# Kernel tuning notes

Hardware: AMD Instinct MI355X
Metric: run time of the kernel (lower is better)

## Reference

```python
import jax, jax.numpy as jnp
import numpy as np

# ---- static config (from init_kwargs) ----
CANVAS = (4, 32, 32)        # (C1, C2, C3) latent video canvas
TILE = (4, 8, 8)            # (T1, T2, T3) tile dims
KERNEL = (1, 3, 3)          # sliding kernel in tile units
ROPE_DIMS = (16, 56, 56)    # per-axis RoPE dims, sums to head_dim
THETA = 256.0
HEADS = 16
HEAD_DIM = 128
HIDDEN = HEADS * HEAD_DIM
B = 1
L = CANVAS[0] * CANVAS[1] * CANVAS[2]
EPS = 1e-6
SCALE = HEAD_DIM ** -0.5
D = tuple(CANVAS[i] // TILE[i] for i in range(3))   # tile grid (D1,D2,D3)
N_TILES = D[0] * D[1] * D[2]
T_TOK = TILE[0] * TILE[1] * TILE[2]


def _rope_tables():
    # 3D meshgrid positions, per-axis 1D rotary tables concatenated on feature dim
    grids = np.meshgrid(*[np.arange(c, dtype=np.float32) for c in CANVAS], indexing='ij')
    cos_l, sin_l = [], []
    for i in range(3):
        dim = ROPE_DIMS[i]
        freqs = 1.0 / (THETA ** (np.arange(0, dim, 2, dtype=np.float32) / dim))
        ang = grids[i].reshape(-1)[:, None] * freqs[None, :]          # [L, dim/2]
        cos_l.append(np.repeat(np.cos(ang), 2, axis=1))               # [L, dim]
        sin_l.append(np.repeat(np.sin(ang), 2, axis=1))
    return jnp.asarray(np.concatenate(cos_l, 1)), jnp.asarray(np.concatenate(sin_l, 1))


def _window_indices():
    # For each query tile (d1,d2,d3): attends to a clamped kernel window of kv tiles
    d1, d2, d3 = np.meshgrid(*[np.arange(d) for d in D], indexing='ij')
    idx = []
    for i, dg in enumerate((d1, d2, d3)):
        k = KERNEL[i]
        s = np.clip(dg - k // 2, 0, D[i] - k)                         # window start, [D1,D2,D3]
        shape = [1, 1, 1]
        shape[i] = k
        idx.append(s[..., None, None, None] + np.arange(k).reshape(shape))
    flat = (idx[0] * D[1] + idx[1]) * D[2] + idx[2]                   # [D1,D2,D3,k1,k2,k3]
    kt = KERNEL[0] * KERNEL[1] * KERNEL[2]
    return jnp.asarray(flat.reshape(N_TILES, kt))


def _tile(x):
    # [B,H,L,E] -> [B,H,N_tiles,T_tok,E] with (D1,T1,D2,T2,D3,T3) -> (D1,D2,D3,T1,T2,T3)
    b, h, _, e = x.shape
    x = x.reshape(b, h, D[0], TILE[0], D[1], TILE[1], D[2], TILE[2], e)
    x = x.transpose(0, 1, 2, 4, 6, 3, 5, 7, 8)
    return x.reshape(b, h, N_TILES, T_TOK, e)


def _untile(x):
    # inverse of _tile: [B,H,N_tiles,T_tok,E] -> [B,H,L,E]
    b, h, _, _, e = x.shape
    x = x.reshape(b, h, D[0], D[1], D[2], TILE[0], TILE[1], TILE[2], e)
    x = x.transpose(0, 1, 2, 5, 3, 6, 4, 7, 8)
    return x.reshape(b, h, L, e)


def _rms(x, g):
    return x * jax.lax.rsqrt(jnp.mean(x * x, axis=-1, keepdims=True) + EPS) * g


def _rope(x, cos, sin):
    # x: [B,L,H,E], cos/sin: [L,E]; rotate-half in interleaved pairs
    xr = x.reshape(*x.shape[:-1], HEAD_DIM // 2, 2)
    rot = jnp.stack([-xr[..., 1], xr[..., 0]], axis=-1).reshape(x.shape)
    return x * cos[None, :, None, :] + rot * sin[None, :, None, :]


def _forward(hidden_states, Wq, bq, Wk, bk, Wv, bv, Wo, bo, gq, gk):
    cos, sin = _rope_tables()
    q = hidden_states @ Wq + bq
    k = hidden_states @ Wk + bk
    v = hidden_states @ Wv + bv
    q = q.reshape(B, L, HEADS, HEAD_DIM)
    k = k.reshape(B, L, HEADS, HEAD_DIM)
    v = v.reshape(B, L, HEADS, HEAD_DIM)
    q = _rope(_rms(q, gq), cos, sin)
    k = _rope(_rms(k, gk), cos, sin)
    q = q.transpose(0, 2, 1, 3)  # [B,H,L,E]
    k = k.transpose(0, 2, 1, 3)
    v = v.transpose(0, 2, 1, 3)
    qt = _tile(q)                # [B,H,N,T,E]
    kt = _tile(k)
    vt = _tile(v)
    win = _window_indices()      # [N, Kt]
    kt_w = kt[:, :, win].reshape(B, HEADS, N_TILES, -1, HEAD_DIM)  # [B,H,N,Kt*T,E]
    vt_w = vt[:, :, win].reshape(B, HEADS, N_TILES, -1, HEAD_DIM)
    s = jnp.einsum('bhnqe,bhnke->bhnqk', qt, kt_w) * SCALE
    p = jax.nn.softmax(s, axis=-1)
    o = jnp.einsum('bhnqk,bhnke->bhnqe', p, vt_w)
    o = _untile(o).transpose(0, 2, 1, 3).reshape(B, L, HIDDEN)
    return o @ Wo + bo


def setup_inputs() -> dict:
    key = jax.random.key(0)
    ks = jax.random.split(key, 6)
    w = 0.02
    return {
        'hidden_states': jax.random.normal(ks[0], (B, L, HIDDEN), jnp.float32),
        'Wq': jax.random.normal(ks[1], (HIDDEN, HIDDEN), jnp.float32) * w,
        'bq': jnp.zeros((HIDDEN,), jnp.float32),
        'Wk': jax.random.normal(ks[2], (HIDDEN, HIDDEN), jnp.float32) * w,
        'bk': jnp.zeros((HIDDEN,), jnp.float32),
        'Wv': jax.random.normal(ks[3], (HIDDEN, HIDDEN), jnp.float32) * w,
        'bv': jnp.zeros((HIDDEN,), jnp.float32),
        'Wo': jax.random.normal(ks[4], (HIDDEN, HIDDEN), jnp.float32) * w,
        'bo': jnp.zeros((HIDDEN,), jnp.float32),
        'gq': jnp.ones((HEAD_DIM,), jnp.float32),
        'gk': jnp.ones((HEAD_DIM,), jnp.float32),
    }


def reference(hidden_states, Wq, bq, Wk, bk, Wv, bv, Wo, bo, gq, gk):
    return _forward(hidden_states, Wq, bq, Wk, bk, Wv, bv, Wo, bo, gq, gk)
```

## Files before the change

### kernel.cpp

```cpp
#include <hip/hip_runtime.h>
#include <math.h>

typedef __attribute__((ext_vector_type(8))) short bf16x8;
typedef __attribute__((ext_vector_type(4))) float f32x4;
typedef unsigned short u16;
typedef unsigned int u32;

#define N_TOK 4096
#define HID   2048
#define N_HEAD 16
#define HDIM  128
#define QK_SCALE 0.08838834764831845f
#define LOG2E_   1.4426950408889634f

__device__ __forceinline__ u16 f2bf(float x) {
  union { float f; u32 u; } v; v.f = x;
  u32 r = v.u + 0x7fffu + ((v.u >> 16) & 1u);
  return (u16)(r >> 16);
}

__device__ __forceinline__ void async16(const void* g, void* l) {
  __builtin_amdgcn_global_load_lds(
      (const __attribute__((address_space(1))) void*)g,
      (__attribute__((address_space(3))) void*)l, 16, 0, 0);
}

#define MFMA(a, b, c) __builtin_amdgcn_mfma_f32_16x16x32_bf16((a), (b), (c), 0, 0, 0)

__global__ void k_rope(float* __restrict__ cosT, float* __restrict__ sinT) {
  int l = blockIdx.x;
  int p = threadIdx.x;
  int c1 = l >> 10, c2 = (l >> 5) & 31, c3 = l & 31;
  int pos, j; float dim;
  if (p < 8)       { pos = c1; j = p;      dim = 16.f; }
  else if (p < 36) { pos = c2; j = p - 8;  dim = 56.f; }
  else             { pos = c3; j = p - 36; dim = 56.f; }
  float freq = exp2f(-8.0f * (2.0f * (float)j) / dim);
  float ang = (float)pos * freq;
  float s, c;
  sincosf(ang, &s, &c);
  cosT[l * 64 + p] = c;
  sinT[l * 64 + p] = s;
}

__global__ __launch_bounds__(256) void k_cvt_x(const float* __restrict__ X, u16* __restrict__ Xb) {
  int i = blockIdx.x * 256 + threadIdx.x;
  float4 v = ((const float4*)X)[i];
  ushort4 o;
  o.x = f2bf(v.x); o.y = f2bf(v.y); o.z = f2bf(v.z); o.w = f2bf(v.w);
  ((ushort4*)Xb)[i] = o;
}

__global__ __launch_bounds__(256) void k_tw(const float* __restrict__ Wq, const float* __restrict__ Wk,
                                            const float* __restrict__ Wv, const float* __restrict__ Wo,
                                            u16* __restrict__ WT) {
  int z = blockIdx.z;
  const float* W = (z == 0) ? Wq : (z == 1) ? Wk : (z == 2) ? Wv : Wo;
  u16* dst = WT + (size_t)z * 2048 * 2048;
  __shared__ __align__(16) float T[64][69];
  int n0 = blockIdx.x * 64, k0 = blockIdx.y * 64;
  int tid = threadIdx.x;
  int r = tid >> 4, c4 = tid & 15;
#pragma unroll
  for (int i = 0; i < 4; ++i) {
    int row = r + i * 16;
    float4 v = *(const float4*)(W + (size_t)(k0 + row) * 2048 + n0 + c4 * 4);
    T[row][c4 * 4 + 0] = v.x; T[row][c4 * 4 + 1] = v.y;
    T[row][c4 * 4 + 2] = v.z; T[row][c4 * 4 + 3] = v.w;
  }
  __syncthreads();
#pragma unroll
  for (int i = 0; i < 4; ++i) {
    int row = r + i * 16;
    ushort4 o;
    o.x = f2bf(T[c4 * 4 + 0][row]);
    o.y = f2bf(T[c4 * 4 + 1][row]);
    o.z = f2bf(T[c4 * 4 + 2][row]);
    o.w = f2bf(T[c4 * 4 + 3][row]);
    *(ushort4*)(dst + (size_t)(n0 + row) * 2048 + k0 + c4 * 4) = o;
  }
}

__global__ __launch_bounds__(256) void k_gemm(const u16* __restrict__ A, const u16* __restrict__ Bt,
                                              const float* __restrict__ bias, float* __restrict__ C,
                                              int M, int N, int K) {
  __shared__ __align__(16) char lds[2][2][16384];
  int nbn = N >> 7;
  int nwg = gridDim.x;
  int wg = (int)blockIdx.x;
  int cpx = nwg >> 3;
  wg = (wg & 7) * cpx + (wg >> 3);
  int bm = wg / nbn, bn = wg - bm * nbn;
  int tid = threadIdx.x;
  int lane = tid & 63, wid = tid >> 6;
  int g = lane >> 4, cl = lane & 15;
  int wm = (wid >> 1) * 64, wn = (wid & 1) * 64;
  const char* Ab0 = (const char*)A + (size_t)bm * 128 * (size_t)(K * 2);
  const char* Bb0 = (const char*)Bt + (size_t)bn * 128 * (size_t)(K * 2);
  int nk = K >> 6;

  f32x4 acc[4][4] = {};

  auto stage = [&](int buf, int kt) {
    const char* Ab = Ab0 + kt * 128;
    const char* Bb = Bb0 + kt * 128;
    char* La = &lds[buf][0][0];
    char* Lb = &lds[buf][1][0];
#pragma unroll
    for (int i = 0; i < 4; ++i) {
      int flat = tid + 256 * i;
      int row = flat >> 3, sb = flat & 7;
      async16(Ab + (size_t)row * (K * 2) + ((sb ^ (row & 7)) << 4), La + flat * 16);
    }
#pragma unroll
    for (int i = 0; i < 4; ++i) {
      int flat = tid + 256 * i;
      int row = flat >> 3, sb = flat & 7;
      async16(Bb + (size_t)row * (K * 2) + ((sb ^ (row & 7)) << 4), Lb + flat * 16);
    }
  };

  stage(0, 0);
  __syncthreads();
  for (int kt = 0; kt < nk; ++kt) {
    int cur = kt & 1;
    if (kt + 1 < nk) stage(cur ^ 1, kt + 1);
    const char* La = &lds[cur][0][0];
    const char* Lb = &lds[cur][1][0];
#pragma unroll
    for (int ks = 0; ks < 2; ++ks) {
      bf16x8 af[4], bfr[4];
#pragma unroll
      for (int mf = 0; mf < 4; ++mf) {
        int row = wm + mf * 16 + cl;
        af[mf] = *(const bf16x8*)(La + row * 128 + (((ks * 4 + g) ^ (row & 7)) << 4));
      }
#pragma unroll
      for (int nf = 0; nf < 4; ++nf) {
        int row = wn + nf * 16 + cl;
        bfr[nf] = *(const bf16x8*)(Lb + row * 128 + (((ks * 4 + g) ^ (row & 7)) << 4));
      }
#pragma unroll
      for (int mf = 0; mf < 4; ++mf)
#pragma unroll
        for (int nf = 0; nf < 4; ++nf)
          acc[mf][nf] = MFMA(af[mf], bfr[nf], acc[mf][nf]);
    }
    __syncthreads();
  }
#pragma unroll
  for (int mf = 0; mf < 4; ++mf)
#pragma unroll
    for (int nf = 0; nf < 4; ++nf) {
      int col = bn * 128 + wn + nf * 16 + cl;
      float b = bias[col];
#pragma unroll
      for (int r = 0; r < 4; ++r) {
        int row = bm * 128 + wm + mf * 16 + g * 4 + r;
        C[(size_t)row * N + col] = acc[mf][nf][r] + b;
      }
    }
}

__global__ __launch_bounds__(256) void k_prep_qk(const float* __restrict__ src, const float* __restrict__ gg,
                                                 const float* __restrict__ cosT, const float* __restrict__ sinT,
                                                 u16* __restrict__ dst, int isk) {
  int job = blockIdx.x * 4 + (threadIdx.x >> 6);
  int lane = threadIdx.x & 63;
  int tok = job & 4095, h = job >> 12;
  const float* row = src + (size_t)tok * 2048 + h * 128;
  float2 x = *(const float2*)(row + lane * 2);
  float ss = x.x * x.x + x.y * x.y;
#pragma unroll
  for (int m = 1; m < 64; m <<= 1) ss += __shfl_xor(ss, m, 64);
  float rms = rsqrtf(ss * (1.0f / 128.0f) + 1e-6f);
  float x0 = x.x * rms * gg[lane * 2];
  float x1 = x.y * rms * gg[lane * 2 + 1];
  float c = cosT[tok * 64 + lane], s = sinT[tok * 64 + lane];
  float y0 = x0 * c - x1 * s;
  float y1 = x1 * c + x0 * s;
  if (!isk) { y0 *= QK_SCALE * LOG2E_; y1 *= QK_SCALE * LOG2E_; }
  u32 pk = (u32)f2bf(y0) | ((u32)f2bf(y1) << 16);
  int c1 = tok >> 10, c2 = (tok >> 5) & 31, c3 = tok & 31;
  int n = (c2 >> 3) * 4 + (c3 >> 3);
  int t = c1 * 64 + (c2 & 7) * 8 + (c3 & 7);
  size_t rowidx = (size_t)(h * 16 + n) * 256 + t;
  if (!isk) {
    ((u32*)dst)[rowidx * 64 + lane] = pk;
  } else {
    char* base = (char*)dst + rowidx * 256;
    *(u32*)(base + ((((lane >> 2) ^ (t & 7)) << 4) + (lane & 3) * 4)) = pk;
  }
}

__global__ __launch_bounds__(256) void k_prep_v(const float* __restrict__ src, u16* __restrict__ Vt) {
  __shared__ __align__(16) u16 T[128][72];
  int tid = threadIdx.x;
  int h = blockIdx.x >> 6, n = (blockIdx.x >> 2) & 15, ch = blockIdx.x & 3;
  int d2 = n >> 2, d3 = n & 3;
  int tc = tid >> 2, cq = tid & 3;
  int tok = (ch * 32 + d2 * 8 + (tc >> 3)) * 32 + d3 * 8 + (tc & 7);
  const float* sp = src + (size_t)tok * 2048 + h * 128;
#pragma unroll
  for (int i = 0; i < 8; ++i) {
    int d0 = cq * 4 + i * 16;
    float4 v = *(const float4*)(sp + d0);
    T[d0 + 0][tc] = f2bf(v.x); T[d0 + 1][tc] = f2bf(v.y);
    T[d0 + 2][tc] = f2bf(v.z); T[d0 + 3][tc] = f2bf(v.w);
  }
  __syncthreads();
  int d = tid >> 1, half = tid & 1;
  char* dstb = (char*)Vt + ((size_t)((h * 16 + n) * 4 + ch) * 128 + d) * 128;
#pragma unroll
  for (int b = 0; b < 4; ++b) {
    int blk = half * 4 + b;
    uint4 val = *(const uint4*)&T[d][blk * 8];
    *(uint4*)(dstb + ((blk ^ (d & 7)) << 4)) = val;
  }
}

__global__ __launch_bounds__(512) void k_attn(const u16* __restrict__ Qt, const u16* __restrict__ Kt,
                                              const u16* __restrict__ Vt, u16* __restrict__ AO) {
  __shared__ __align__(16) char Kl[2][16384];
  __shared__ __align__(16) char Vl[2][16384];
  __shared__ __align__(16) char Pl[8][4096];
  int tid = threadIdx.x;
  int lane = tid & 63, wid = tid >> 6;
  int g = lane >> 4, cl = lane & 15;
  int h = blockIdx.x >> 4, n = blockIdx.x & 15;
  int d2 = n >> 2, d3 = n & 3;
  int s2 = d2 - 1; s2 = s2 < 0 ? 0 : (s2 > 1 ? 1 : s2);
  int s3 = d3 - 1; s3 = s3 < 0 ? 0 : (s3 > 1 ? 1 : s3);
  int q0 = wid * 32;

  bf16x8 qf[2][4];
  const char* Qb = (const char*)Qt + (size_t)(h * 16 + n) * 256 * 256;
#pragma unroll
  for (int nq = 0; nq < 2; ++nq)
#pragma unroll
    for (int kf = 0; kf < 4; ++kf)
      qf[nq][kf] = *(const bf16x8*)(Qb + (q0 + nq * 16 + cl) * 256 + kf * 64 + g * 16);

  f32x4 o[2][8] = {};
  float ms0 = -__builtin_inff(), ms1 = -__builtin_inff();
  float ls0 = 0.f, ls1 = 0.f;

  auto stage = [&](int buf, int c) {
    int kvi = c >> 2, cc = c & 3;
    int i2 = kvi / 3, i3 = kvi - i2 * 3;
    int kvt = (s2 + i2) * 4 + (s3 + i3);
    const char* Kb = (const char*)Kt + ((size_t)((h * 16 + kvt) * 256 + cc * 64)) * 256;
    const char* Vb = (const char*)Vt + ((size_t)((h * 16 + kvt) * 4 + cc)) * 16384;
#pragma unroll
    for (int i = 0; i < 2; ++i) {
      int flat = tid + 512 * i;
      async16(Kb + flat * 16, &Kl[buf][0] + flat * 16);
      async16(Vb + flat * 16, &Vl[buf][0] + flat * 16);
    }
  };

  stage(0, 0);
  __syncthreads();

  char* Pw = &Pl[wid][0];
  for (int c = 0; c < 36; ++c) {
    int cur = c & 1;
    if (c + 1 < 36) stage(cur ^ 1, c + 1);
    const char* Kc = &Kl[cur][0];
    f32x4 st[4][2] = {};
#pragma unroll
    for (int ks = 0; ks < 4; ++ks) {
      bf16x8 af[4];
#pragma unroll
      for (int mk = 0; mk < 4; ++mk) {
        int row = mk * 16 + cl;
        af[mk] = *(const bf16x8*)(Kc + row * 256 + (((ks * 4 + g) ^ (row & 7)) << 4));
      }
#pragma unroll
      for (int mk = 0; mk < 4; ++mk) {
        st[mk][0] = MFMA(af[mk], qf[0][ks], st[mk][0]);
        st[mk][1] = MFMA(af[mk], qf[1][ks], st[mk][1]);
      }
    }
    float al0, al1;
    {
      float cm = st[0][0][0];
#pragma unroll
      for (int mk = 0; mk < 4; ++mk)
#pragma unroll
        for (int r = 0; r < 4; ++r) cm = fmaxf(cm, st[mk][0][r]);
      cm = fmaxf(cm, __shfl_xor(cm, 16, 64));
      cm = fmaxf(cm, __shfl_xor(cm, 32, 64));
      float mn = fmaxf(ms0, cm);
      al0 = exp2f(ms0 - mn);
      float rs = 0.f;
#pragma unroll
      for (int mk = 0; mk < 4; ++mk)
#pragma unroll
        for (int r = 0; r < 4; ++r) {
          float p = exp2f(st[mk][0][r] - mn);
          st[mk][0][r] = p; rs += p;
        }
      rs += __shfl_xor(rs, 16, 64);
      rs += __shfl_xor(rs, 32, 64);
      ls0 = ls0 * al0 + rs; ms0 = mn;
    }
    {
      float cm = st[0][1][0];
#pragma unroll
      for (int mk = 0; mk < 4; ++mk)
#pragma unroll
        for (int r = 0; r < 4; ++r) cm = fmaxf(cm, st[mk][1][r]);
      cm = fmaxf(cm, __shfl_xor(cm, 16, 64));
      cm = fmaxf(cm, __shfl_xor(cm, 32, 64));
      float mn = fmaxf(ms1, cm);
      al1 = exp2f(ms1 - mn);
      float rs = 0.f;
#pragma unroll
      for (int mk = 0; mk < 4; ++mk)
#pragma unroll
        for (int r = 0; r < 4; ++r) {
          float p = exp2f(st[mk][1][r] - mn);
          st[mk][1][r] = p; rs += p;
        }
      rs += __shfl_xor(rs, 16, 64);
      rs += __shfl_xor(rs, 32, 64);
      ls1 = ls1 * al1 + rs; ms1 = mn;
    }
#pragma unroll
    for (int nq = 0; nq < 2; ++nq) {
      int q = nq * 16 + cl;
#pragma unroll
      for (int mk = 0; mk < 4; ++mk)
#pragma unroll
        for (int rp = 0; rp < 2; ++rp) {
          u32 pk = (u32)f2bf(st[mk][nq][rp * 2]) | ((u32)f2bf(st[mk][nq][rp * 2 + 1]) << 16);
          int kv = mk * 16 + g * 4 + rp * 2;
          *(u32*)(Pw + q * 128 + (((kv >> 3) ^ (q & 7)) << 4) + (kv & 7) * 2) = pk;
        }
    }
    float ar0[4], ar1[4];
#pragma unroll
    for (int r = 0; r < 4; ++r) {
      ar0[r] = __shfl(al0, g * 4 + r, 64);
      ar1[r] = __shfl(al1, g * 4 + r, 64);
    }
#pragma unroll
    for (int nd = 0; nd < 8; ++nd)
#pragma unroll
      for (int r = 0; r < 4; ++r) {
        o[0][nd][r] *= ar0[r];
        o[1][nd][r] *= ar1[r];
      }
    const char* Vc = &Vl[cur][0];
#pragma unroll
    for (int ks = 0; ks < 2; ++ks) {
      bf16x8 pf0, pf1, vf[8];
      {
        int q = cl;
        pf0 = *(const bf16x8*)(Pw + q * 128 + (((ks * 4 + g) ^ (q & 7)) << 4));
        q = 16 + cl;
        pf1 = *(const bf16x8*)(Pw + q * 128 + (((ks * 4 + g) ^ (q & 7)) << 4));
      }
#pragma unroll
      for (int nd = 0; nd < 8; ++nd) {
        int d = nd * 16 + cl;
        vf[nd] = *(const bf16x8*)(Vc + d * 128 + (((ks * 4 + g) ^ (d & 7)) << 4));
      }
#pragma unroll
      for (int nd = 0; nd < 8; ++nd) {
        o[0][nd] = MFMA(pf0, vf[nd], o[0][nd]);
        o[1][nd] = MFMA(pf1, vf[nd], o[1][nd]);
      }
    }
    __syncthreads();
  }
  float lr0[4], lr1[4];
#pragma unroll
  for (int r = 0; r < 4; ++r) {
    lr0[r] = 1.0f / __shfl(ls0, g * 4 + r, 64);
    lr1[r] = 1.0f / __shfl(ls1, g * 4 + r, 64);
  }
#pragma unroll
  for (int mo = 0; mo < 2; ++mo)
#pragma unroll
    for (int r = 0; r < 4; ++r) {
      int t = q0 + mo * 16 + g * 4 + r;
      int t1 = t >> 6, t2 = (t >> 3) & 7, t3 = t & 7;
      int tok = (t1 * 32 + d2 * 8 + t2) * 32 + d3 * 8 + t3;
      u16* orow = AO + (size_t)tok * HID + h * HDIM;
      float lr = (mo == 0) ? lr0[r] : lr1[r];
#pragma unroll
      for (int nd = 0; nd < 8; ++nd)
        orow[nd * 16 + cl] = f2bf(o[mo][nd][r] * lr);
    }
}

extern "C" void kernel_launch(void* const* d_in, const int* in_sizes, int n_in,
                              void* d_out, int out_size, void* d_ws, size_t ws_size,
                              hipStream_t stream) {
  const float* X  = (const float*)d_in[0];
  const float* Wq = (const float*)d_in[1];
  const float* bq = (const float*)d_in[2];
  const float* Wk = (const float*)d_in[3];
  const float* bk = (const float*)d_in[4];
  const float* Wv = (const float*)d_in[5];
  const float* bv = (const float*)d_in[6];
  const float* Wo = (const float*)d_in[7];
  const float* bo = (const float*)d_in[8];
  const float* gq = (const float*)d_in[9];
  const float* gk = (const float*)d_in[10];

  char* ws = (char*)d_ws;
  size_t off = 0;
  auto alloc = [&](size_t bytes) { void* p = ws + off; off = (off + bytes + 255) & ~(size_t)255; return p; };
  u16*   Xb   = (u16*)alloc((size_t)N_TOK * HID * 2);
  u16*   WT   = (u16*)alloc((size_t)4 * 2048 * 2048 * 2);
  float* PF   = (float*)alloc((size_t)N_TOK * HID * 4);
  float* COS  = (float*)alloc((size_t)N_TOK * 64 * 4);
  float* SIN  = (float*)alloc((size_t)N_TOK * 64 * 4);
  u16*   Qt   = (u16*)alloc((size_t)N_TOK * HID * 2);
  u16*   Kt   = (u16*)alloc((size_t)N_TOK * HID * 2);
  u16*   Vt   = (u16*)alloc((size_t)N_TOK * HID * 2);
  u16*   AO   = (u16*)alloc((size_t)N_TOK * HID * 2);
  float* OUT  = (float*)d_out;

  k_rope<<<N_TOK, 64, 0, stream>>>(COS, SIN);
  k_cvt_x<<<(N_TOK * HID / 4) / 256, 256, 0, stream>>>(X, Xb);
  k_tw<<<dim3(32, 32, 4), 256, 0, stream>>>(Wq, Wk, Wv, Wo, WT);

  k_gemm<<<512, 256, 0, stream>>>(Xb, WT + (size_t)0 * 2048 * 2048, bq, PF, 4096, 2048, 2048);
  k_prep_qk<<<16384, 256, 0, stream>>>(PF, gq, COS, SIN, Qt, 0);
  k_gemm<<<512, 256, 0, stream>>>(Xb, WT + (size_t)1 * 2048 * 2048, bk, PF, 4096, 2048, 2048);
  k_prep_qk<<<16384, 256, 0, stream>>>(PF, gk, COS, SIN, Kt, 1);
  k_gemm<<<512, 256, 0, stream>>>(Xb, WT + (size_t)2 * 2048 * 2048, bv, PF, 4096, 2048, 2048);
  k_prep_v<<<1024, 256, 0, stream>>>(PF, Vt);

  k_attn<<<256, 512, 0, stream>>>(Qt, Kt, Vt, AO);

  k_gemm<<<512, 256, 0, stream>>>(AO, WT + (size_t)3 * 2048 * 2048, bo, OUT, 4096, 2048, 2048);
}
```

Measured before the change: 450.5 us.

## Fuse QKV into pipelined 256x256 GEMM and simplify attention softmax

Measured after the change: 460.8 us. +2.3%, slower.

```diff
diff --git a/kernel.cpp b/kernel.cpp
--- a/kernel.cpp
+++ b/kernel.cpp
@@ -17,6 +17,12 @@
   union { float f; u32 u; } v; v.f = x;
   u32 r = v.u + 0x7fffu + ((v.u >> 16) & 1u);
   return (u16)(r >> 16);
+}
+
+__device__ __forceinline__ u32 cvtpk(float lo, float hi) {
+  u32 r;
+  asm("v_cvt_pk_bf16_f32 %0, %1, %2" : "=v"(r) : "v"(lo), "v"(hi));
+  return r;
 }
 
 __device__ __forceinline__ void async16(const void* g, void* l) {
@@ -81,94 +87,127 @@
   }
 }
 
-__global__ __launch_bounds__(256) void k_gemm(const u16* __restrict__ A, const u16* __restrict__ Bt,
-                                              const float* __restrict__ bias, float* __restrict__ C,
-                                              int M, int N, int K) {
-  __shared__ __align__(16) char lds[2][2][16384];
-  int nbn = N >> 7;
+
+#define VM8 asm volatile("s_waitcnt vmcnt(8)" ::: "memory");
+#define VM6 asm volatile("s_waitcnt vmcnt(6)" ::: "memory");
+#define VMNONE
+
+#define STAGEU(SB, SAB, SH, ST) do {                                            \
+    int st_ = (ST) < Tk ? (ST) : Tk - 1;                                        \
+    const char* src_ = ((SAB) ? Bp : Ap) + (size_t)((SH) * 128) * Kb + (size_t)st_ * 128; \
+    char* dstl_ = &Lds[SB][SAB][SH][0];                                         \
+    _Pragma("unroll")                                                           \
+    for (int i_ = 0; i_ < 2; ++i_) {                                            \
+      int flat_ = tid + 512 * i_;                                               \
+      int row_ = flat_ >> 3, sb_ = flat_ & 7;                                   \
+      async16(src_ + (size_t)row_ * Kb + ((sb_ ^ (row_ & 7)) << 4), dstl_ + flat_ * 16); \
+    }                                                                           \
+  } while (0)
+
+#define PHASE(BUF, MH, NH, READA, VMOP, SB, SAB, SH, ST) do {                   \
+    VMOP                                                                        \
+    __builtin_amdgcn_s_barrier();                                               \
+    asm volatile("" ::: "memory");                                              \
+    bf16x8 bb[2][2];                                                            \
+    const char* Lm = &Lds[BUF][0][MH][0];                                       \
+    const char* Ln = &Lds[BUF][1][NH][0];                                       \
+    if (READA) {                                                                \
+      _Pragma("unroll")                                                         \
+      for (int kk = 0; kk < 2; ++kk)                                            \
+        _Pragma("unroll")                                                       \
+        for (int mf = 0; mf < 4; ++mf) {                                        \
+          int row = wmIdx * 64 + mf * 16 + cl;                                  \
+          af[kk][mf] = *(const bf16x8*)(Lm + row * 128 + (((kk * 4 + g) ^ (row & 7)) << 4)); \
+        }                                                                       \
+    }                                                                           \
+    _Pragma("unroll")                                                           \
+    for (int kk = 0; kk < 2; ++kk)                                              \
+      _Pragma("unroll")                                                         \
+      for (int nf = 0; nf < 2; ++nf) {                                          \
+        int row = wnIdx * 32 + nf * 16 + cl;                                    \
+        bb[kk][nf] = *(const bf16x8*)(Ln + row * 128 + (((kk * 4 + g) ^ (row & 7)) << 4)); \
+      }                                                                         \
+    STAGEU(SB, SAB, SH, ST);                                                    \
+    __builtin_amdgcn_s_setprio(1);                                              \
+    _Pragma("unroll")                                                           \
+    for (int kk = 0; kk < 2; ++kk)                                              \
+      _Pragma("unroll")                                                         \
+      for (int mf = 0; mf < 4; ++mf)                                            \
+        _Pragma("unroll")                                                       \
+        for (int nf = 0; nf < 2; ++nf)                                          \
+          acc[(MH) * 4 + mf][(NH) * 2 + nf] =                                   \
+              MFMA(af[kk][mf], bb[kk][nf], acc[(MH) * 4 + mf][(NH) * 2 + nf]);  \
+    __builtin_amdgcn_s_setprio(0);                                              \
+  } while (0)
+
+__global__ __launch_bounds__(512, 2) void k_gemm8(const u16* __restrict__ A, const u16* __restrict__ Bt,
+                                                  const float* __restrict__ b0, const float* __restrict__ b1,
+                                                  const float* __restrict__ b2, float* __restrict__ C,
+                                                  int gn, int K, int ldc) {
+  __shared__ __align__(16) char Lds[2][2][2][16384];
+  int tid = threadIdx.x;
+  int lane = tid & 63, wid = tid >> 6;
+  int g = lane >> 4, cl = lane & 15;
+  int wmIdx = wid >> 2, wnIdx = wid & 3;
   int nwg = gridDim.x;
   int wg = (int)blockIdx.x;
   int cpx = nwg >> 3;
   wg = (wg & 7) * cpx + (wg >> 3);
-  int bm = wg / nbn, bn = wg - bm * nbn;
-  int tid = threadIdx.x;
-  int lane = tid & 63, wid = tid >> 6;
-  int g = lane >> 4, cl = lane & 15;
-  int wm = (wid >> 1) * 64, wn = (wid & 1) * 64;
-  const char* Ab0 = (const char*)A + (size_t)bm * 128 * (size_t)(K * 2);
-  const char* Bb0 = (const char*)Bt + (size_t)bn * 128 * (size_t)(K * 2);
-  int nk = K >> 6;
-
-  f32x4 acc[4][4] = {};
-
-  auto stage = [&](int buf, int kt) {
-    const char* Ab = Ab0 + kt * 128;
-    const char* Bb = Bb0 + kt * 128;
-    char* La = &lds[buf][0][0];
-    char* Lb = &lds[buf][1][0];
-#pragma unroll
-    for (int i = 0; i < 4; ++i) {
-      int flat = tid + 256 * i;
-      int row = flat >> 3, sb = flat & 7;
-      async16(Ab + (size_t)row * (K * 2) + ((sb ^ (row & 7)) << 4), La + flat * 16);
-    }
-#pragma unroll
-    for (int i = 0; i < 4; ++i) {
-      int flat = tid + 256 * i;
-      int row = flat >> 3, sb = flat & 7;
-      async16(Bb + (size_t)row * (K * 2) + ((sb ^ (row & 7)) << 4), Lb + flat * 16);
-    }
-  };
-
-  stage(0, 0);
-  __syncthreads();
-  for (int kt = 0; kt < nk; ++kt) {
-    int cur = kt & 1;
-    if (kt + 1 < nk) stage(cur ^ 1, kt + 1);
-    const char* La = &lds[cur][0][0];
-    const char* Lb = &lds[cur][1][0];
-#pragma unroll
-    for (int ks = 0; ks < 2; ++ks) {
-      bf16x8 af[4], bfr[4];
-#pragma unroll
-      for (int mf = 0; mf < 4; ++mf) {
-        int row = wm + mf * 16 + cl;
-        af[mf] = *(const bf16x8*)(La + row * 128 + (((ks * 4 + g) ^ (row & 7)) << 4));
-      }
-#pragma unroll
-      for (int nf = 0; nf < 4; ++nf) {
-        int row = wn + nf * 16 + cl;
-        bfr[nf] = *(const bf16x8*)(Lb + row * 128 + (((ks * 4 + g) ^ (row & 7)) << 4));
-      }
-#pragma unroll
-      for (int mf = 0; mf < 4; ++mf)
-#pragma unroll
-        for (int nf = 0; nf < 4; ++nf)
-          acc[mf][nf] = MFMA(af[mf], bfr[nf], acc[mf][nf]);
-    }
-    __syncthreads();
-  }
-#pragma unroll
-  for (int mf = 0; mf < 4; ++mf)
-#pragma unroll
-    for (int nf = 0; nf < 4; ++nf) {
-      int col = bn * 128 + wn + nf * 16 + cl;
-      float b = bias[col];
-#pragma unroll
-      for (int r = 0; r < 4; ++r) {
-        int row = bm * 128 + wm + mf * 16 + g * 4 + r;
-        C[(size_t)row * N + col] = acc[mf][nf][r] + b;
-      }
-    }
-}
-
-__global__ __launch_bounds__(256) void k_prep_qk(const float* __restrict__ src, const float* __restrict__ gg,
+  int bm = wg / gn, bn = wg % gn;
+  size_t Kb = (size_t)K * 2;
+  const char* Ap = (const char*)A + (size_t)bm * 256 * Kb;
+  const char* Bp = (const char*)Bt + (size_t)bn * 256 * Kb;
+  int Tk = K >> 6;
+
+  f32x4 acc[8][4] = {};
+  bf16x8 af[2][4];
+
+  STAGEU(0, 0, 0, 0);
+  STAGEU(0, 1, 0, 0);
+  STAGEU(0, 0, 1, 0);
+  STAGEU(0, 1, 1, 0);
+  STAGEU(1, 0, 0, 1);
+  STAGEU(1, 1, 0, 1);
+
+  int nIter = Tk >> 1;
+  for (int it = 0; it < nIter; ++it) {
+    int t = 2 * it;
+    PHASE(0, 0, 0, 1, VM8,    1, 0, 1, t + 1);
+    PHASE(0, 0, 1, 0, VM6,    1, 1, 1, t + 1);
+    PHASE(0, 1, 0, 1, VMNONE, 0, 0, 0, t + 2);
+    PHASE(0, 1, 1, 0, VMNONE, 0, 1, 0, t + 2);
+    PHASE(1, 0, 0, 1, VM8,    0, 0, 1, t + 2);
+    PHASE(1, 0, 1, 0, VM6,    0, 1, 1, t + 2);
+    PHASE(1, 1, 0, 1, VMNONE, 1, 0, 0, t + 3);
+    PHASE(1, 1, 1, 0, VMNONE, 1, 1, 0, t + 3);
+  }
+
+#pragma unroll
+  for (int mfp = 0; mfp < 8; ++mfp) {
+    int rowBase = (mfp < 4 ? wmIdx * 64 + mfp * 16 : 128 + wmIdx * 64 + (mfp - 4) * 16) + g * 4;
+    int rowG = bm * 256 + rowBase;
+#pragma unroll
+    for (int nfp = 0; nfp < 4; ++nfp) {
+      int colLoc = (nfp < 2 ? wnIdx * 32 + nfp * 16 : 128 + wnIdx * 32 + (nfp - 2) * 16) + cl;
+      int col = bn * 256 + colLoc;
+      int z = col >> 11;
+      const float* bp = (z == 0) ? b0 : (z == 1) ? b1 : b2;
+      float bv = bp[col & 2047];
+#pragma unroll
+      for (int rr = 0; rr < 4; ++rr)
+        C[(size_t)(rowG + rr) * ldc + col] = acc[mfp][nfp][rr] + bv;
+    }
+  }
+}
+
+__global__ __launch_bounds__(256) void k_prep_qk(const float* __restrict__ src, int stride,
+                                                 const float* __restrict__ gg,
                                                  const float* __restrict__ cosT, const float* __restrict__ sinT,
                                                  u16* __restrict__ dst, int isk) {
   int job = blockIdx.x * 4 + (threadIdx.x >> 6);
   int lane = threadIdx.x & 63;
   int tok = job & 4095, h = job >> 12;
-  const float* row = src + (size_t)tok * 2048 + h * 128;
+  const float* row = src + (size_t)tok * stride + h * 128;
   float2 x = *(const float2*)(row + lane * 2);
   float ss = x.x * x.x + x.y * x.y;
 #pragma unroll
@@ -180,7 +219,7 @@
   float y0 = x0 * c - x1 * s;
   float y1 = x1 * c + x0 * s;
   if (!isk) { y0 *= QK_SCALE * LOG2E_; y1 *= QK_SCALE * LOG2E_; }
-  u32 pk = (u32)f2bf(y0) | ((u32)f2bf(y1) << 16);
+  u32 pk = cvtpk(y0, y1);
   int c1 = tok >> 10, c2 = (tok >> 5) & 31, c3 = tok & 31;
   int n = (c2 >> 3) * 4 + (c3 >> 3);
   int t = c1 * 64 + (c2 & 7) * 8 + (c3 & 7);
@@ -193,14 +232,15 @@
   }
 }
 
-__global__ __launch_bounds__(256) void k_prep_v(const float* __restrict__ src, u16* __restrict__ Vt) {
+__global__ __launch_bounds__(256) void k_prep_v(const float* __restrict__ src, int stride,
+                                                u16* __restrict__ Vt) {
   __shared__ __align__(16) u16 T[128][72];
   int tid = threadIdx.x;
   int h = blockIdx.x >> 6, n = (blockIdx.x >> 2) & 15, ch = blockIdx.x & 3;
   int d2 = n >> 2, d3 = n & 3;
   int tc = tid >> 2, cq = tid & 3;
   int tok = (ch * 32 + d2 * 8 + (tc >> 3)) * 32 + d3 * 8 + (tc & 7);
-  const float* sp = src + (size_t)tok * 2048 + h * 128;
+  const float* sp = src + (size_t)tok * stride + h * 128;
 #pragma unroll
   for (int i = 0; i < 8; ++i) {
     int d0 = cq * 4 + i * 16;
@@ -227,7 +267,10 @@
   int tid = threadIdx.x;
   int lane = tid & 63, wid = tid >> 6;
   int g = lane >> 4, cl = lane & 15;
-  int h = blockIdx.x >> 4, n = blockIdx.x & 15;
+  int bid = (int)blockIdx.x;
+  int xcd = bid & 7, i = bid >> 3;
+  int h = xcd * 2 + (i >> 4);
+  int n = i & 15;
   int d2 = n >> 2, d3 = n & 3;
   int s2 = d2 - 1; s2 = s2 < 0 ? 0 : (s2 > 1 ? 1 : s2);
   int s3 = d3 - 1; s3 = s3 < 0 ? 0 : (s3 > 1 ? 1 : s3);
@@ -242,8 +285,7 @@
       qf[nq][kf] = *(const bf16x8*)(Qb + (q0 + nq * 16 + cl) * 256 + kf * 64 + g * 16);
 
   f32x4 o[2][8] = {};
-  float ms0 = -__builtin_inff(), ms1 = -__builtin_inff();
-  float ls0 = 0.f, ls1 = 0.f;
+  float L0 = 0.f, L1 = 0.f;
 
   auto stage = [&](int buf, int c) {
     int kvi = c >> 2, cc = c & 3;
@@ -252,8 +294,8 @@
     const char* Kb = (const char*)Kt + ((size_t)((h * 16 + kvt) * 256 + cc * 64)) * 256;
     const char* Vb = (const char*)Vt + ((size_t)((h * 16 + kvt) * 4 + cc)) * 16384;
 #pragma unroll
-    for (int i = 0; i < 2; ++i) {
-      int flat = tid + 512 * i;
+    for (int i_ = 0; i_ < 2; ++i_) {
+      int flat = tid + 512 * i_;
       async16(Kb + flat * 16, &Kl[buf][0] + flat * 16);
       async16(Vb + flat * 16, &Vl[buf][0] + flat * 16);
     }
@@ -268,6 +310,7 @@
     if (c + 1 < 36) stage(cur ^ 1, c + 1);
     const char* Kc = &Kl[cur][0];
     f32x4 st[4][2] = {};
+    __builtin_amdgcn_s_setprio(1);
 #pragma unroll
     for (int ks = 0; ks < 4; ++ks) {
       bf16x8 af[4];
@@ -282,51 +325,16 @@
         st[mk][1] = MFMA(af[mk], qf[1][ks], st[mk][1]);
       }
     }
-    float al0, al1;
-    {
-      float cm = st[0][0][0];
-#pragma unroll
-      for (int mk = 0; mk < 4; ++mk)
-#pragma unroll
-        for (int r = 0; r < 4; ++r) cm = fmaxf(cm, st[mk][0][r]);
-      cm = fmaxf(cm, __shfl_xor(cm, 16, 64));
-      cm = fmaxf(cm, __shfl_xor(cm, 32, 64));
-      float mn = fmaxf(ms0, cm);
-      al0 = exp2f(ms0 - mn);
-      float rs = 0.f;
-#pragma unroll
-      for (int mk = 0; mk < 4; ++mk)
-#pragma unroll
-        for (int r = 0; r < 4; ++r) {
-          float p = exp2f(st[mk][0][r] - mn);
-          st[mk][0][r] = p; rs += p;
-        }
-      rs += __shfl_xor(rs, 16, 64);
-      rs += __shfl_xor(rs, 32, 64);
-      ls0 = ls0 * al0 + rs; ms0 = mn;
-    }
-    {
-      float cm = st[0][1][0];
-#pragma unroll
-      for (int mk = 0; mk < 4; ++mk)
-#pragma unroll
-        for (int r = 0; r < 4; ++r) cm = fmaxf(cm, st[mk][1][r]);
-      cm = fmaxf(cm, __shfl_xor(cm, 16, 64));
-      cm = fmaxf(cm, __shfl_xor(cm, 32, 64));
-      float mn = fmaxf(ms1, cm);
-      al1 = exp2f(ms1 - mn);
-      float rs = 0.f;
-#pragma unroll
-      for (int mk = 0; mk < 4; ++mk)
-#pragma unroll
-        for (int r = 0; r < 4; ++r) {
-          float p = exp2f(st[mk][1][r] - mn);
-          st[mk][1][r] = p; rs += p;
-        }
-      rs += __shfl_xor(rs, 16, 64);
-      rs += __shfl_xor(rs, 32, 64);
-      ls1 = ls1 * al1 + rs; ms1 = mn;
-    }
+    __builtin_amdgcn_s_setprio(0);
+#pragma unroll
+    for (int mk = 0; mk < 4; ++mk)
+#pragma unroll
+      for (int r = 0; r < 4; ++r) {
+        float p0 = exp2f(st[mk][0][r]);
+        float p1 = exp2f(st[mk][1][r]);
+        st[mk][0][r] = p0; L0 += p0;
+        st[mk][1][r] = p1; L1 += p1;
+      }
 #pragma unroll
     for (int nq = 0; nq < 2; ++nq) {
       int q = nq * 16 + cl;
@@ -334,25 +342,13 @@
       for (int mk = 0; mk < 4; ++mk)
 #pragma unroll
         for (int rp = 0; rp < 2; ++rp) {
-          u32 pk = (u32)f2bf(st[mk][nq][rp * 2]) | ((u32)f2bf(st[mk][nq][rp * 2 + 1]) << 16);
+          u32 pk = cvtpk(st[mk][nq][rp * 2], st[mk][nq][rp * 2 + 1]);
           int kv = mk * 16 + g * 4 + rp * 2;
           *(u32*)(Pw + q * 128 + (((kv >> 3) ^ (q & 7)) << 4) + (kv & 7) * 2) = pk;
         }
     }
-    float ar0[4], ar1[4];
-#pragma unroll
-    for (int r = 0; r < 4; ++r) {
-      ar0[r] = __shfl(al0, g * 4 + r, 64);
-      ar1[r] = __shfl(al1, g * 4 + r, 64);
-    }
-#pragma unroll
-    for (int nd = 0; nd < 8; ++nd)
-#pragma unroll
-      for (int r = 0; r < 4; ++r) {
-        o[0][nd][r] *= ar0[r];
-        o[1][nd][r] *= ar1[r];
-      }
     const char* Vc = &Vl[cur][0];
+    __builtin_amdgcn_s_setprio(1);
 #pragma unroll
     for (int ks = 0; ks < 2; ++ks) {
       bf16x8 pf0, pf1, vf[8];
@@ -373,13 +369,16 @@
         o[1][nd] = MFMA(pf1, vf[nd], o[1][nd]);
       }
     }
+    __builtin_amdgcn_s_setprio(0);
     __syncthreads();
   }
+  L0 += __shfl_xor(L0, 16, 64); L0 += __shfl_xor(L0, 32, 64);
+  L1 += __shfl_xor(L1, 16, 64); L1 += __shfl_xor(L1, 32, 64);
   float lr0[4], lr1[4];
 #pragma unroll
   for (int r = 0; r < 4; ++r) {
-    lr0[r] = 1.0f / __shfl(ls0, g * 4 + r, 64);
-    lr1[r] = 1.0f / __shfl(ls1, g * 4 + r, 64);
+    lr0[r] = 1.0f / __shfl(L0, g * 4 + r, 64);
+    lr1[r] = 1.0f / __shfl(L1, g * 4 + r, 64);
   }
 #pragma unroll
   for (int mo = 0; mo < 2; ++mo)
@@ -414,29 +413,40 @@
   char* ws = (char*)d_ws;
   size_t off = 0;
   auto alloc = [&](size_t bytes) { void* p = ws + off; off = (off + bytes + 255) & ~(size_t)255; return p; };
-  u16*   Xb   = (u16*)alloc((size_t)N_TOK * HID * 2);
-  u16*   WT   = (u16*)alloc((size_t)4 * 2048 * 2048 * 2);
-  float* PF   = (float*)alloc((size_t)N_TOK * HID * 4);
-  float* COS  = (float*)alloc((size_t)N_TOK * 64 * 4);
-  float* SIN  = (float*)alloc((size_t)N_TOK * 64 * 4);
-  u16*   Qt   = (u16*)alloc((size_t)N_TOK * HID * 2);
-  u16*   Kt   = (u16*)alloc((size_t)N_TOK * HID * 2);
-  u16*   Vt   = (u16*)alloc((size_t)N_TOK * HID * 2);
-  u16*   AO   = (u16*)alloc((size_t)N_TOK * HID * 2);
-  float* OUT  = (float*)d_out;
+
+  u16*   Xb  = (u16*)alloc((size_t)N_TOK * HID * 2);
+  u16*   WT  = (u16*)alloc((size_t)4 * 2048 * 2048 * 2);
+  float* COS = (float*)alloc((size_t)N_TOK * 64 * 4);
+  float* SIN = (float*)alloc((size_t)N_TOK * 64 * 4);
+  u16*   Qt  = (u16*)alloc((size_t)N_TOK * HID * 2);
+  u16*   Kt  = (u16*)alloc((size_t)N_TOK * HID * 2);
+  u16*   Vt  = (u16*)alloc((size_t)N_TOK * HID * 2);
+  u16*   AO  = (u16*)alloc((size_t)N_TOK * HID * 2);
+  size_t fixed = off;
+  size_t needF = fixed + (size_t)N_TOK * 6144 * 4 + 256;
+  bool fused = (ws_size >= needF);
+  float* PF = (float*)alloc(fused ? (size_t)N_TOK * 6144 * 4 : (size_t)N_TOK * 2048 * 4);
+  float* OUT = (float*)d_out;
 
   k_rope<<<N_TOK, 64, 0, stream>>>(COS, SIN);
   k_cvt_x<<<(N_TOK * HID / 4) / 256, 256, 0, stream>>>(X, Xb);
   k_tw<<<dim3(32, 32, 4), 256, 0, stream>>>(Wq, Wk, Wv, Wo, WT);
 
-  k_gemm<<<512, 256, 0, stream>>>(Xb, WT + (size_t)0 * 2048 * 2048, bq, PF, 4096, 2048, 2048);
-  k_prep_qk<<<16384, 256, 0, stream>>>(PF, gq, COS, SIN, Qt, 0);
-  k_gemm<<<512, 256, 0, stream>>>(Xb, WT + (size_t)1 * 2048 * 2048, bk, PF, 4096, 2048, 2048);
-  k_prep_qk<<<16384, 256, 0, stream>>>(PF, gk, COS, SIN, Kt, 1);
-  k_gemm<<<512, 256, 0, stream>>>(Xb, WT + (size_t)2 * 2048 * 2048, bv, PF, 4096, 2048, 2048);
-  k_prep_v<<<1024, 256, 0, stream>>>(PF, Vt);
+  if (fused) {
+    k_gemm8<<<16 * 24, 512, 0, stream>>>(Xb, WT, bq, bk, bv, PF, 24, 2048, 6144);
+    k_prep_qk<<<16384, 256, 0, stream>>>(PF + 0,    6144, gq, COS, SIN, Qt, 0);
+    k_prep_qk<<<16384, 256, 0, stream>>>(PF + 2048, 6144, gk, COS, SIN, Kt, 1);
+    k_prep_v <<<1024,  256, 0, stream>>>(PF + 4096, 6144, Vt);
+  } else {
+    k_gemm8<<<16 * 8, 512, 0, stream>>>(Xb, WT + (size_t)0 * 2048 * 2048, bq, bq, bq, PF, 8, 2048, 2048);
+    k_prep_qk<<<16384, 256, 0, stream>>>(PF, 2048, gq, COS, SIN, Qt, 0);
+    k_gemm8<<<16 * 8, 512, 0, stream>>>(Xb, WT + (size_t)1 * 2048 * 2048, bk, bk, bk, PF, 8, 2048, 2048);
+    k_prep_qk<<<16384, 256, 0, stream>>>(PF, 2048, gk, COS, SIN, Kt, 1);
+    k_gemm8<<<16 * 8, 512, 0, stream>>>(Xb, WT + (size_t)2 * 2048 * 2048, bv, bv, bv, PF, 8, 2048, 2048);
+    k_prep_v<<<1024, 256, 0, stream>>>(PF, 2048, Vt);
+  }
 
   k_attn<<<256, 512, 0, stream>>>(Qt, Kt, Vt, AO);
 
-  k_gemm<<<512, 256, 0, stream>>>(AO, WT + (size_t)3 * 2048 * 2048, bo, OUT, 4096, 2048, 2048);
-}
+  k_gemm8<<<16 * 8, 512, 0, stream>>>(AO, WT + (size_t)3 * 2048 * 2048, bo, bo, bo, OUT, 8, 2048, 2048);
+}
```
